# Performance work log

Measured on AMD Instinct MI355X. Metric: run time of the kernel, lower is better.

## Reference

```python
import jax, jax.numpy as jnp
import numpy as np
from jax import lax

V, D, H, L, K = 50257, 1024, 2048, 6, 3
B, S = 4, 2048
EPS = 1.1920929e-07  # torch.finfo(float32).eps (torch RMSNorm default eps=None)


def rmsnorm(x, w):
    return x * lax.rsqrt(jnp.mean(x * x, axis=-1, keepdims=True) + EPS) * w


def depthwise_conv(x, w, b):
    # x: (B,S,D), w: (D,1,K) depthwise kernel, padding='same' as in torch Conv1d
    y = lax.conv_general_dilated(x.transpose(0, 2, 1), w, (1,), 'SAME',
                                 dimension_numbers=('NCH', 'OIH', 'NCH'),
                                 feature_group_count=x.shape[-1])
    return y.transpose(0, 2, 1) + b


def mingru(x, h0, wz, bz, wh, bh, wo, bo):
    # minGRU: z=sigmoid(Wz x), h_tilde=Wh x, h_t=(1-z_t)h_{t-1}+z_t h_tilde_t (parallel scan)
    z = jax.nn.sigmoid(jnp.einsum('bsd,hd->bsh', x, wz) + bz)
    htil = jnp.einsum('bsd,hd->bsh', x, wh) + bh
    a, bc = 1.0 - z, z * htil

    def comb(c1, c2):
        a1, b1 = c1
        a2, b2 = c2
        return a1 * a2, a2 * b1 + b2

    A, Bc = lax.associative_scan(comb, (a, bc), axis=1)
    h = A * h0[:, None, :] + Bc                      # (B,S,H)
    out = jnp.einsum('bsh,dh->bsd', h, wo) + bo      # project back to model dim
    return out, h[:, -1]


def setup_inputs():
    key = jax.random.key(0)
    ks = jax.random.split(key, 16)
    sc = 0.02
    p = {}
    p['x'] = jax.random.randint(ks[0], (B, S), 0, V)
    p['h_prev'] = jax.random.normal(ks[1], (B, L, H), jnp.float32)
    p['emb'] = jax.random.normal(ks[2], (V, D), jnp.float32) * sc
    p['conv_dw_w'] = jax.random.normal(ks[3], (L, D, 1, K), jnp.float32) * sc
    p['conv_dw_b'] = jnp.zeros((L, D), jnp.float32)
    p['conv_pw_w'] = jax.random.normal(ks[4], (L, D, D), jnp.float32) * sc
    p['conv_pw_b'] = jnp.zeros((L, D), jnp.float32)
    p['n1_w'] = jnp.ones((L, D), jnp.float32)
    p['wz'] = jax.random.normal(ks[5], (L, H, D), jnp.float32) * sc
    p['bz'] = jnp.zeros((L, H), jnp.float32)
    p['wh'] = jax.random.normal(ks[6], (L, H, D), jnp.float32) * sc
    p['bh'] = jnp.zeros((L, H), jnp.float32)
    p['wo'] = jax.random.normal(ks[7], (L, D, H), jnp.float32) * sc
    p['bo'] = jnp.zeros((L, D), jnp.float32)
    p['n2_w'] = jnp.ones((L, D), jnp.float32)
    p['f1_w'] = jax.random.normal(ks[8], (L, H, D), jnp.float32) * sc
    p['f1_b'] = jnp.zeros((L, H), jnp.float32)
    p['f2_w'] = jax.random.normal(ks[9], (L, D, H), jnp.float32) * sc
    p['f2_b'] = jnp.zeros((L, D), jnp.float32)
    p['norm_w'] = jnp.ones((D,), jnp.float32)
    p['out_w'] = jax.random.normal(ks[10], (H, D), jnp.float32) * sc
    p['out_b'] = jnp.zeros((H,), jnp.float32)
    return p


def reference(x, h_prev, emb, conv_dw_w, conv_dw_b, conv_pw_w, conv_pw_b, n1_w,
              wz, bz, wh, bh, wo, bo, n2_w, f1_w, f1_b, f2_w, f2_b,
              norm_w, out_w, out_b):
    xe = emb[x]                                      # (B,S,D)
    h_next = []
    for l in range(L):
        c = depthwise_conv(xe, conv_dw_w[l], conv_dw_b[l])
        c = jnp.einsum('bsd,ed->bse', c, conv_pw_w[l]) + conv_pw_b[l]  # 1x1 conv
        xe = c + xe
        g, hl = mingru(rmsnorm(xe, n1_w[l]), h_prev[:, l],
                       wz[l], bz[l], wh[l], bh[l], wo[l], bo[l])
        xe = g + xe
        f = rmsnorm(xe, n2_w[l])
        f = jnp.einsum('bsd,hd->bsh', f, f1_w[l]) + f1_b[l]
        f = jax.nn.gelu(f, approximate=False)
        f = jnp.einsum('bsh,dh->bsd', f, f2_w[l]) + f2_b[l]
        xe = f + xe
        h_next.append(hl)
    out = jnp.einsum('bsd,hd->bsh', rmsnorm(xe, norm_w), out_w) + out_b
    return out, jnp.stack(h_next, axis=1)             # (B,S,H), (B,L,H)
```

## Files before the change

kernel.cpp:

```cpp
#include <hip/hip_runtime.h>

typedef __bf16 bf16x8 __attribute__((ext_vector_type(8)));
typedef float f32x4 __attribute__((ext_vector_type(4)));

#define DEVI __device__ __forceinline__

namespace {
constexpr int cB = 4, cS = 2048, cD = 1024, cH = 2048, cL = 6;
constexpr int cM = cB * cS;
constexpr float cEPS = 1.1920929e-07f;
constexpr int NCH = 16, CHS = cS / NCH;
}

DEVI unsigned short f2bf(float f) {
  union { float f; unsigned u; } c; c.f = f;
  const unsigned u = c.u;
  return (unsigned short)((u + 0x7fffu + ((u >> 16) & 1u)) >> 16);
}
DEVI float bf2f(unsigned short h) {
  union { unsigned u; float f; } c; c.u = ((unsigned)h) << 16;
  return c.f;
}

DEVI void gld16(const void* g, void* l) {
  __builtin_amdgcn_global_load_lds(
      (__attribute__((address_space(1))) void*)g,
      (__attribute__((address_space(3))) void*)l, 16, 0, 0);
}

union F4 { float4 v; float a[4]; };

__global__ __launch_bounds__(256) void embed_k(const int* __restrict__ x,
    const float* __restrict__ emb, float* __restrict__ xe) {
  const int bs = blockIdx.x;
  const int idx = x[bs];
  const int t = threadIdx.x;
  *(float4*)&xe[(size_t)bs * cD + t * 4] =
      *(const float4*)&emb[(size_t)idx * cD + t * 4];
}

__global__ __launch_bounds__(256) void dwconv_k(const float* __restrict__ xe,
    const float* __restrict__ w, const float* __restrict__ bias,
    unsigned short* __restrict__ out) {
  const int bs = blockIdx.x;
  const int s = bs & (cS - 1);
  const int t = threadIdx.x;
  const int d = t * 4;
  const size_t base = (size_t)bs * cD + d;
  F4 x0, xm, xp, vb;
  x0.v = *(const float4*)&xe[base];
  xm.v = make_float4(0.f, 0.f, 0.f, 0.f);
  xp.v = make_float4(0.f, 0.f, 0.f, 0.f);
  if (s > 0) xm.v = *(const float4*)&xe[base - cD];
  if (s < cS - 1) xp.v = *(const float4*)&xe[base + cD];
  vb.v = *(const float4*)&bias[d];
  unsigned short o[4];
#pragma unroll
  for (int j = 0; j < 4; ++j) {
    const float w0 = w[(d + j) * 3 + 0];
    const float w1 = w[(d + j) * 3 + 1];
    const float w2 = w[(d + j) * 3 + 2];
    o[j] = f2bf(xm.a[j] * w0 + x0.a[j] * w1 + xp.a[j] * w2 + vb.a[j]);
  }
  *(ushort4*)&out[base] = make_ushort4(o[0], o[1], o[2], o[3]);
}

__global__ __launch_bounds__(256) void rmsnorm_k(const float* __restrict__ x,
    const float* __restrict__ w, unsigned short* __restrict__ o) {
  const int row = blockIdx.x;
  const int t = threadIdx.x;
  const size_t base = (size_t)row * cD + t * 4;
  F4 v; v.v = *(const float4*)&x[base];
  float ss = v.a[0]*v.a[0] + v.a[1]*v.a[1] + v.a[2]*v.a[2] + v.a[3]*v.a[3];
#pragma unroll
  for (int off = 32; off > 0; off >>= 1) ss += __shfl_down(ss, off, 64);
  __shared__ float red[4];
  if ((t & 63) == 0) red[t >> 6] = ss;
  __syncthreads();
  const float scale = rsqrtf((red[0]+red[1]+red[2]+red[3]) * (1.f/cD) + cEPS);
  F4 wv; wv.v = *(const float4*)&w[t * 4];
  *(ushort4*)&o[base] = make_ushort4(
      f2bf(v.a[0]*scale*wv.a[0]), f2bf(v.a[1]*scale*wv.a[1]),
      f2bf(v.a[2]*scale*wv.a[2]), f2bf(v.a[3]*scale*wv.a[3]));
}

__global__ __launch_bounds__(256) void cvt_k(const float* __restrict__ s,
    unsigned short* __restrict__ d, int n) {
  const int i = (blockIdx.x * 256 + threadIdx.x) * 4;
  if (i >= n) return;
  F4 v; v.v = *(const float4*)&s[i];
  *(ushort4*)&d[i] = make_ushort4(f2bf(v.a[0]), f2bf(v.a[1]),
                                  f2bf(v.a[2]), f2bf(v.a[3]));
}

template<int N, int K, int EPI>
__global__ __launch_bounds__(256) void gemm_bt(
    const unsigned short* __restrict__ A, const unsigned short* __restrict__ W,
    const float* __restrict__ bias, float* __restrict__ Cf,
    unsigned short* __restrict__ Cb) {
  __shared__ unsigned short As[128 * 32];
  __shared__ unsigned short Bs[128 * 32];
  const int t = threadIdx.x;
  const int lane = t & 63;
  const int wave = t >> 6;
  const int m0 = blockIdx.x * 128;
  const int n0 = blockIdx.y * 128;
  const int wm = (wave >> 1) * 64;
  const int wn = (wave & 1) * 64;
  const int fr = lane & 15;
  const int fk = (lane >> 4) * 8;

  const int arow = t >> 2;
  const int acol = (t & 3) * 8;
  const unsigned short* gA = A + (size_t)(m0 + arow) * K + acol;
  const unsigned short* gB = W + (size_t)(n0 + arow) * K + acol;
  unsigned short* lA = As + wave * 512;
  unsigned short* lB = Bs + wave * 512;

  f32x4 acc[4][4] = {};
  for (int k0 = 0; k0 < K; k0 += 32) {
    gld16(gA + k0, lA);
    gld16(gA + k0 + (size_t)64 * K, lA + 2048);
    gld16(gB + k0, lB);
    gld16(gB + k0 + (size_t)64 * K, lB + 2048);
    __syncthreads();
    bf16x8 fa[4], fb[4];
#pragma unroll
    for (int i = 0; i < 4; ++i) {
      fa[i] = *(const bf16x8*)&As[(wm + i * 16 + fr) * 32 + fk];
      fb[i] = *(const bf16x8*)&Bs[(wn + i * 16 + fr) * 32 + fk];
    }
#pragma unroll
    for (int i = 0; i < 4; ++i)
#pragma unroll
      for (int j = 0; j < 4; ++j)
        acc[i][j] = __builtin_amdgcn_mfma_f32_16x16x32_bf16(
            fa[i], fb[j], acc[i][j], 0, 0, 0);
    __syncthreads();
  }

  const int r0 = m0 + wm + ((lane >> 4) << 2);
  const int c0 = n0 + wn + fr;
#pragma unroll
  for (int i = 0; i < 4; ++i)
#pragma unroll
    for (int j = 0; j < 4; ++j) {
      const int col = c0 + j * 16;
      const float bv = bias[col];
#pragma unroll
      for (int r = 0; r < 4; ++r) {
        const size_t idx = (size_t)(r0 + i * 16 + r) * N + col;
        const float v = acc[i][j][r] + bv;
        if constexpr (EPI == 1) {
          Cf[idx] += v;
        } else {
          Cf[idx] = v;
        }
      }
    }
}

#define RDA(BUF, MH)                                                        \
  _Pragma("unroll") for (int mf = 0; mf < 4; ++mf)                          \
  _Pragma("unroll") for (int kk = 0; kk < 2; ++kk)                          \
      a[mf * 2 + kk] = *(const bf16x8*)&lds[(BUF)*16384 + aB + (MH)*4096 +  \
                                            mf * 1024 + kk * 32];

#define RDB(BUF)                                                            \
  _Pragma("unroll") for (int q = 0; q < 4; ++q)                             \
  _Pragma("unroll") for (int kk = 0; kk < 2; ++kk)                          \
      b[q >> 1][(q & 1) * 2 + kk] =                                         \
          *(const bf16x8*)&lds[(BUF)*16384 + bB + q * 1024 + kk * 32];

#define MMQ(MH, NH)                                                         \
  _Pragma("unroll") for (int mf = 0; mf < 4; ++mf)                          \
  _Pragma("unroll") for (int nf = 0; nf < 2; ++nf)                          \
  _Pragma("unroll") for (int kk = 0; kk < 2; ++kk)                          \
      acc[(MH)*4 + mf][(NH)*2 + nf] = __builtin_amdgcn_mfma_f32_16x16x32_bf16( \
          a[mf * 2 + kk], b[NH][nf * 2 + kk], acc[(MH)*4 + mf][(NH)*2 + nf],  \
          0, 0, 0);

#define PH_SYNC()                                                           \
  __builtin_amdgcn_s_barrier();                                             \
  asm volatile("s_waitcnt lgkmcnt(0)" ::: "memory");                        \
  __builtin_amdgcn_sched_barrier(0);                                        \
  __builtin_amdgcn_s_setprio(1)

#define PH_END()                                                            \
  __builtin_amdgcn_s_setprio(0);                                            \
  __builtin_amdgcn_s_barrier()

#define TILE_PHASES(TI, BUF, OBUF)                                          \
  {                                                                         \
    RDA(BUF, 0); RDB(BUF);                                                  \
    { const int n1 = (TI) + 1;                                              \
      stA((n1 < NT) ? n1 : 0, 1, (n1 < NT) ? ldsA(OBUF, 1) : ldsDummy); }   \
    asm volatile("s_waitcnt lgkmcnt(8)" ::: "memory");                      \
    PH_SYNC(); MMQ(0, 0); PH_END();                                         \
    { const int n2 = (TI) + 2;                                              \
      stB((n2 < NT) ? n2 : 0, 0, (n2 < NT) ? ldsB(BUF, 0) : ldsDummy); }    \
    PH_SYNC(); MMQ(0, 1); PH_END();                                         \
    RDA(BUF, 1);                                                            \
    { const int n2 = (TI) + 2;                                              \
      stB((n2 < NT) ? n2 : 0, 1, (n2 < NT) ? ldsB(BUF, 1) : ldsDummy); }    \
    PH_SYNC(); MMQ(1, 1); PH_END();                                         \
    { const int n2 = (TI) + 2;                                              \
      stA((n2 < NT) ? n2 : 0, 0, (n2 < NT) ? ldsA(BUF, 0) : ldsDummy); }    \
    asm volatile("s_waitcnt vmcnt(6)" ::: "memory");                        \
    PH_SYNC(); MMQ(1, 0); PH_END();                                         \
  }

template<int N, int K, int EPI, int NS>
__global__ __launch_bounds__(512, 2) void gemm8p(
    const unsigned short* __restrict__ A,
    const unsigned short* __restrict__ W0,
    const unsigned short* __restrict__ W1,
    const float* __restrict__ bias0, const float* __restrict__ bias1,
    float* __restrict__ Cf, unsigned short* __restrict__ Cb,
    unsigned short* __restrict__ Cb2) {
  static_assert(K % 128 == 0, "NT must be even");
  constexpr int NT = K / 64;
  __shared__ unsigned short lds[73728];
  const int t = threadIdx.x;
  const int lane = t & 63;
  const int wave = t >> 6;
  const int wr = wave >> 2;
  const int wc = wave & 3;
  const int m0 = blockIdx.x * 256;
  const int n0 = blockIdx.y * 256;

  const bool zpart = (n0 < NS);
  const unsigned short* Wp = zpart ? W0 : W1;
  const int nw0 = zpart ? n0 : n0 - NS;
  const float* bp = zpart ? bias0 : bias1;
  const int CW = zpart ? NS : (N - NS);

  const int srow = t >> 3;
  const int scol = ((t & 7) * 8) ^ (((t >> 5) & 1) << 4);
  const unsigned short* gA = A  + (size_t)(m0 + srow) * K + scol;
  const unsigned short* gB = Wp + (size_t)(nw0 + srow) * K + scol;
  const int ldsw = wave * 512;

  auto ldsA = [&](int buf, int h) -> unsigned short* {
    return (unsigned short*)&lds[buf * 16384 + h * 8192 + ldsw];
  };
  auto ldsB = [&](int buf, int h) -> unsigned short* {
    return (unsigned short*)&lds[32768 + buf * 16384 + h * 8192 + ldsw];
  };
  unsigned short* ldsDummy = (unsigned short*)&lds[65536 + ldsw];
  auto stA = [&](int tile, int h, unsigned short* dst) {
    const unsigned short* s = gA + (size_t)(h * 128) * K + tile * 64;
    gld16(s, dst);
    gld16(s + (size_t)64 * K, dst + 4096);
  };
  auto stB = [&](int tile, int h, unsigned short* dst) {
    const unsigned short* s = gB + (size_t)(h * 128) * K + tile * 64;
    gld16(s, dst);
    gld16(s + (size_t)64 * K, dst + 4096);
  };

  const int sx = ((lane >> 2) & 1) << 4;
  const int aoff = (lane & 15) * 64 + (((lane >> 4) * 8) ^ sx);
  const int aB = wr * 8192 + aoff;
  const int bB = 32768 + (wc >> 1) * 8192 + (wc & 1) * 4096 + aoff;

  bf16x8 a[8];
  bf16x8 b[2][4];
  f32x4 acc[8][4] = {};

  stB(0, 0, ldsB(0, 0)); stB(0, 1, ldsB(0, 1));
  stA(0, 0, ldsA(0, 0)); stA(0, 1, ldsA(0, 1));
  stB(1, 0, ldsB(1, 0)); stB(1, 1, ldsB(1, 1));
  stA(1, 0, ldsA(1, 0));
  asm volatile("s_waitcnt vmcnt(6)" ::: "memory");
  __builtin_amdgcn_s_barrier();

  for (int tp = 0; tp < NT / 2; ++tp) {
    const int t0 = 2 * tp;
    TILE_PHASES(t0, 0, 1);
    TILE_PHASES(t0 + 1, 1, 0);
  }

  float* cf = Cf;
  unsigned short* cb = zpart ? Cb : Cb2;
  const int r0 = m0 + wr * 128 + ((lane >> 4) << 2);
  const int c0 = nw0 + wc * 64 + (lane & 15);
#pragma unroll
  for (int mfg = 0; mfg < 8; ++mfg) {
#pragma unroll
    for (int nfg = 0; nfg < 4; ++nfg) {
      const int col = c0 + nfg * 16;
      const float bv = bp[col];
#pragma unroll
      for (int r = 0; r < 4; ++r) {
        const size_t idx = (size_t)(r0 + mfg * 16 + r) * CW + col;
        const float v = acc[mfg][nfg][r] + bv;
        if constexpr (EPI == 0) {
          cf[idx] = v;
        } else if constexpr (EPI == 4) {
          cb[idx] = f2bf(0.5f * v * (1.f + erff(v * 0.70710678118654752f)));
        } else {
          if (zpart) cb[idx] = f2bf(1.f / (1.f + __expf(-v)));
          else       cb[idx] = f2bf(v);
        }
      }
    }
  }
}

__global__ __launch_bounds__(256) void scan1_k(const unsigned short* __restrict__ z,
    const unsigned short* __restrict__ ht, float* __restrict__ Ac,
    float* __restrict__ Bc) {
  const int tid = blockIdx.x * 256 + threadIdx.x;
  const int hp = (tid & (cH / 2 - 1)) * 2;
  const int ck = (tid / (cH / 2)) & (NCH - 1);
  const int b = tid / ((cH / 2) * NCH);
  const size_t base = ((size_t)b * cS + (size_t)ck * CHS) * cH + hp;
  float a0 = 1.f, s0 = 0.f, a1 = 1.f, s1 = 0.f;
#pragma unroll 4
  for (int s = 0; s < CHS; ++s) {
    const unsigned zz = *(const unsigned*)&z[base + (size_t)s * cH];
    const unsigned hh = *(const unsigned*)&ht[base + (size_t)s * cH];
    const float z0 = bf2f((unsigned short)(zz & 0xffff)), z1 = bf2f((unsigned short)(zz >> 16));
    const float t0 = bf2f((unsigned short)(hh & 0xffff)), t1 = bf2f((unsigned short)(hh >> 16));
    const float aa0 = 1.f - z0, aa1 = 1.f - z1;
    s0 = aa0 * s0 + z0 * t0; a0 *= aa0;
    s1 = aa1 * s1 + z1 * t1; a1 *= aa1;
  }
  const size_t so = ((size_t)b * NCH + ck) * cH + hp;
  *(float2*)&Ac[so] = make_float2(a0, a1);
  *(float2*)&Bc[so] = make_float2(s0, s1);
}

__global__ __launch_bounds__(256) void scan2_k(const float* __restrict__ Ac,
    const float* __restrict__ Bc, const float* __restrict__ h_prev,
    float* __restrict__ P, float* __restrict__ hn, int l) {
  const int tid = blockIdx.x * 256 + threadIdx.x;
  const int h = tid & (cH - 1);
  const int b = tid >> 11;
  float run = h_prev[((size_t)b * cL + l) * cH + h];
#pragma unroll
  for (int c = 0; c < NCH; ++c) {
    const size_t so = ((size_t)b * NCH + c) * cH + h;
    P[so] = run;
    run = Ac[so] * run + Bc[so];
  }
  hn[((size_t)b * cL + l) * cH + h] = run;
}

__global__ __launch_bounds__(256) void scan3_k(const unsigned short* __restrict__ z,
    unsigned short* __restrict__ ht, const float* __restrict__ P) {
  const int tid = blockIdx.x * 256 + threadIdx.x;
  const int hp = (tid & (cH / 2 - 1)) * 2;
  const int ck = (tid / (cH / 2)) & (NCH - 1);
  const int b = tid / ((cH / 2) * NCH);
  const size_t base = ((size_t)b * cS + (size_t)ck * CHS) * cH + hp;
  const size_t so = ((size_t)b * NCH + ck) * cH + hp;
  const float2 rr = *(const float2*)&P[so];
  float r0 = rr.x, r1 = rr.y;
#pragma unroll 4
  for (int s = 0; s < CHS; ++s) {
    const unsigned zz = *(const unsigned*)&z[base + (size_t)s * cH];
    const unsigned hh = *(const unsigned*)&ht[base + (size_t)s * cH];
    const float z0 = bf2f((unsigned short)(zz & 0xffff)), z1 = bf2f((unsigned short)(zz >> 16));
    const float t0 = bf2f((unsigned short)(hh & 0xffff)), t1 = bf2f((unsigned short)(hh >> 16));
    r0 = (1.f - z0) * r0 + z0 * t0;
    r1 = (1.f - z1) * r1 + z1 * t1;
    *(unsigned*)&ht[base + (size_t)s * cH] =
        (unsigned)f2bf(r0) | ((unsigned)f2bf(r1) << 16);
  }
}

extern "C" void kernel_launch(void* const* d_in, const int* in_sizes, int n_in,
                              void* d_out, int out_size, void* d_ws, size_t ws_size,
                              hipStream_t stream) {
  (void)in_sizes; (void)n_in; (void)out_size; (void)ws_size;
  const int*   x      = (const int*)d_in[0];
  const float* h_prev = (const float*)d_in[1];
  const float* emb    = (const float*)d_in[2];
  const float* cdw_w  = (const float*)d_in[3];
  const float* cdw_b  = (const float*)d_in[4];
  const float* cpw_w  = (const float*)d_in[5];
  const float* cpw_b  = (const float*)d_in[6];
  const float* n1w    = (const float*)d_in[7];
  const float* wzp    = (const float*)d_in[8];
  const float* bzp    = (const float*)d_in[9];
  const float* whp    = (const float*)d_in[10];
  const float* bhp    = (const float*)d_in[11];
  const float* wop    = (const float*)d_in[12];
  const float* bop    = (const float*)d_in[13];
  const float* n2w    = (const float*)d_in[14];
  const float* f1wp   = (const float*)d_in[15];
  const float* f1bp   = (const float*)d_in[16];
  const float* f2wp   = (const float*)d_in[17];
  const float* f2bp   = (const float*)d_in[18];
  const float* nw     = (const float*)d_in[19];
  const float* owp    = (const float*)d_in[20];
  const float* obp    = (const float*)d_in[21];

  float* out_main = (float*)d_out;
  float* out_hn   = out_main + (size_t)cM * cH;

  char* p = (char*)d_ws;
  auto alloc = [&](size_t bytes) {
    char* r = p; p += (bytes + 255) & ~(size_t)255; return r;
  };
  float*          xe = (float*)alloc((size_t)cM * cD * 4);
  unsigned short* xn = (unsigned short*)alloc((size_t)cM * cD * 2);
  unsigned short* zb = (unsigned short*)alloc((size_t)cM * cH * 2);
  unsigned short* hb = (unsigned short*)alloc((size_t)cM * cH * 2);
  float* Ac = (float*)alloc((size_t)cB * NCH * cH * 4);
  float* Bc = (float*)alloc((size_t)cB * NCH * cH * 4);
  float* Pr = (float*)alloc((size_t)cB * NCH * cH * 4);
  unsigned short* w_pw = (unsigned short*)alloc((size_t)cL * cD * cD * 2);
  unsigned short* w_z  = (unsigned short*)alloc((size_t)cL * cH * cD * 2);
  unsigned short* w_h  = (unsigned short*)alloc((size_t)cL * cH * cD * 2);
  unsigned short* w_o  = (unsigned short*)alloc((size_t)cL * cD * cH * 2);
  unsigned short* w_f1 = (unsigned short*)alloc((size_t)cL * cH * cD * 2);
  unsigned short* w_f2 = (unsigned short*)alloc((size_t)cL * cD * cH * 2);
  unsigned short* w_ow = (unsigned short*)alloc((size_t)cH * cD * 2);

  auto cvt = [&](const float* src, unsigned short* dst, size_t n) {
    cvt_k<<<dim3((unsigned)(n / 1024)), 256, 0, stream>>>(src, dst, (int)n);
  };

  cvt(cpw_w, w_pw, (size_t)cL * cD * cD);
  cvt(wzp,  w_z,  (size_t)cL * cH * cD);
  cvt(whp,  w_h,  (size_t)cL * cH * cD);
  cvt(wop,  w_o,  (size_t)cL * cD * cH);
  cvt(f1wp, w_f1, (size_t)cL * cH * cD);
  cvt(f2wp, w_f2, (size_t)cL * cD * cH);
  cvt(owp,  w_ow, (size_t)cH * cD);

  embed_k<<<cM, 256, 0, stream>>>(x, emb, xe);

  for (int l = 0; l < cL; ++l) {
    const size_t oDD = (size_t)l * cD * cD, oHD = (size_t)l * cH * cD;

    dwconv_k<<<cM, 256, 0, stream>>>(xe, cdw_w + (size_t)l * cD * 3,
                                     cdw_b + (size_t)l * cD, xn);
    gemm_bt<cD, cD, 1><<<dim3(cM / 128, cD / 128), 256, 0, stream>>>(
        xn, w_pw + oDD, cpw_b + (size_t)l * cD, xe, nullptr);

    rmsnorm_k<<<cM, 256, 0, stream>>>(xe, n1w + (size_t)l * cD, xn);
    gemm8p<2 * cH, cD, 5, cH><<<dim3(cM / 256, 2 * cH / 256), 512, 0, stream>>>(
        xn, w_z + oHD, w_h + oHD, bzp + (size_t)l * cH, bhp + (size_t)l * cH,
        nullptr, zb, hb);
    scan1_k<<<cB * NCH * (cH / 2) / 256, 256, 0, stream>>>(zb, hb, Ac, Bc);
    scan2_k<<<cB * cH / 256, 256, 0, stream>>>(Ac, Bc, h_prev, Pr, out_hn, l);
    scan3_k<<<cB * NCH * (cH / 2) / 256, 256, 0, stream>>>(zb, hb, Pr);
    gemm_bt<cD, cH, 1><<<dim3(cM / 128, cD / 128), 256, 0, stream>>>(
        hb, w_o + oHD, bop + (size_t)l * cD, xe, nullptr);

    rmsnorm_k<<<cM, 256, 0, stream>>>(xe, n2w + (size_t)l * cD, xn);
    gemm8p<cH, cD, 4, cH><<<dim3(cM / 256, cH / 256), 512, 0, stream>>>(
        xn, w_f1 + oHD, w_f1 + oHD, f1bp + (size_t)l * cH, f1bp + (size_t)l * cH,
        nullptr, zb, zb);
    gemm_bt<cD, cH, 1><<<dim3(cM / 128, cD / 128), 256, 0, stream>>>(
        zb, w_f2 + oHD, f2bp + (size_t)l * cD, xe, nullptr);
  }

  rmsnorm_k<<<cM, 256, 0, stream>>>(xe, nw, xn);
  gemm8p<cH, cD, 0, cH><<<dim3(cM / 256, cH / 256), 512, 0, stream>>>(
      xn, w_ow, w_ow, obp, obp, out_main, nullptr, nullptr);
}
```

Measured before the change: 2.359 ms.

## Peel GEMM tail tiles, stage bf16 epilogue through LDS, fuse scan passes

The 256x256 GEMM main loop now peels its last two tiles so out-of-range prefetches into a dummy LDS region are no longer issued. This shrinks shared memory and splits the B-fragment reads across phases. The bf16 epilogues write through swizzled LDS and then issue coalesced 16-byte global stores instead of scattered 2-byte stores. The scan's carry-propagation and apply kernels are merged: each chunk thread recomputes its prefix from the per-chunk A/B summaries, which removes one launch and the P buffer at the cost of redundant serial prefix work. The reordered prologue loads and changed wait counts must still match the pipeline's outstanding-load accounting.

```diff
diff --git a/kernel.cpp b/kernel.cpp
--- a/kernel.cpp
+++ b/kernel.cpp
@@ -166,10 +166,15 @@
       a[mf * 2 + kk] = *(const bf16x8*)&lds[(BUF)*16384 + aB + (MH)*4096 +  \
                                             mf * 1024 + kk * 32];
 
-#define RDB(BUF)                                                            \
-  _Pragma("unroll") for (int q = 0; q < 4; ++q)                             \
+#define RDB0(BUF)                                                           \
+  _Pragma("unroll") for (int q = 0; q < 2; ++q)                             \
   _Pragma("unroll") for (int kk = 0; kk < 2; ++kk)                          \
-      b[q >> 1][(q & 1) * 2 + kk] =                                         \
+      b[0][q * 2 + kk] = *(const bf16x8*)&lds[(BUF)*16384 + bB + q * 1024 + kk * 32];
+
+#define RDB1(BUF)                                                           \
+  _Pragma("unroll") for (int q = 2; q < 4; ++q)                             \
+  _Pragma("unroll") for (int kk = 0; kk < 2; ++kk)                          \
+      b[1][(q & 1) * 2 + kk] =                                              \
           *(const bf16x8*)&lds[(BUF)*16384 + bB + q * 1024 + kk * 32];
 
 #define MMQ(MH, NH)                                                         \
@@ -190,23 +195,19 @@
   __builtin_amdgcn_s_setprio(0);                                            \
   __builtin_amdgcn_s_barrier()
 
-#define TILE_PHASES(TI, BUF, OBUF)                                          \
+#define TILE_PHASES(TI, BUF, OBUF, S1, S2, VM)                              \
   {                                                                         \
-    RDA(BUF, 0); RDB(BUF);                                                  \
-    { const int n1 = (TI) + 1;                                              \
-      stA((n1 < NT) ? n1 : 0, 1, (n1 < NT) ? ldsA(OBUF, 1) : ldsDummy); }   \
-    asm volatile("s_waitcnt lgkmcnt(8)" ::: "memory");                      \
+    RDA(BUF, 0); RDB0(BUF);                                                 \
+    if (S1) { stA((TI) + 1, 1, ldsA(OBUF, 1)); }                            \
     PH_SYNC(); MMQ(0, 0); PH_END();                                         \
-    { const int n2 = (TI) + 2;                                              \
-      stB((n2 < NT) ? n2 : 0, 0, (n2 < NT) ? ldsB(BUF, 0) : ldsDummy); }    \
+    RDB1(BUF);                                                              \
     PH_SYNC(); MMQ(0, 1); PH_END();                                         \
     RDA(BUF, 1);                                                            \
-    { const int n2 = (TI) + 2;                                              \
-      stB((n2 < NT) ? n2 : 0, 1, (n2 < NT) ? ldsB(BUF, 1) : ldsDummy); }    \
+    if (S2) { stB((TI) + 2, 0, ldsB(BUF, 0)); }                             \
     PH_SYNC(); MMQ(1, 1); PH_END();                                         \
-    { const int n2 = (TI) + 2;                                              \
-      stA((n2 < NT) ? n2 : 0, 0, (n2 < NT) ? ldsA(BUF, 0) : ldsDummy); }    \
-    asm volatile("s_waitcnt vmcnt(6)" ::: "memory");                        \
+    if (S2) { stB((TI) + 2, 1, ldsB(BUF, 1)); stA((TI) + 2, 0, ldsA(BUF, 0)); } \
+    if (VM == 6) { asm volatile("s_waitcnt vmcnt(6)" ::: "memory"); }       \
+    else         { asm volatile("s_waitcnt vmcnt(0)" ::: "memory"); }       \
     PH_SYNC(); MMQ(1, 0); PH_END();                                         \
   }
 
@@ -220,7 +221,7 @@
     unsigned short* __restrict__ Cb2) {
   static_assert(K % 128 == 0, "NT must be even");
   constexpr int NT = K / 64;
-  __shared__ unsigned short lds[73728];
+  __shared__ unsigned short lds[65536];
   const int t = threadIdx.x;
   const int lane = t & 63;
   const int wave = t >> 6;
@@ -247,7 +248,6 @@
   auto ldsB = [&](int buf, int h) -> unsigned short* {
     return (unsigned short*)&lds[32768 + buf * 16384 + h * 8192 + ldsw];
   };
-  unsigned short* ldsDummy = (unsigned short*)&lds[65536 + ldsw];
   auto stA = [&](int tile, int h, unsigned short* dst) {
     const unsigned short* s = gA + (size_t)(h * 128) * K + tile * 64;
     gld16(s, dst);
@@ -268,42 +268,65 @@
   bf16x8 b[2][4];
   f32x4 acc[8][4] = {};
 
+  stA(0, 0, ldsA(0, 0)); stA(0, 1, ldsA(0, 1));
   stB(0, 0, ldsB(0, 0)); stB(0, 1, ldsB(0, 1));
-  stA(0, 0, ldsA(0, 0)); stA(0, 1, ldsA(0, 1));
+  stA(1, 0, ldsA(1, 0));
   stB(1, 0, ldsB(1, 0)); stB(1, 1, ldsB(1, 1));
-  stA(1, 0, ldsA(1, 0));
   asm volatile("s_waitcnt vmcnt(6)" ::: "memory");
   __builtin_amdgcn_s_barrier();
 
-  for (int tp = 0; tp < NT / 2; ++tp) {
+  for (int tp = 0; tp < NT / 2 - 1; ++tp) {
     const int t0 = 2 * tp;
-    TILE_PHASES(t0, 0, 1);
-    TILE_PHASES(t0 + 1, 1, 0);
-  }
-
-  float* cf = Cf;
-  unsigned short* cb = zpart ? Cb : Cb2;
-  const int r0 = m0 + wr * 128 + ((lane >> 4) << 2);
-  const int c0 = nw0 + wc * 64 + (lane & 15);
-#pragma unroll
-  for (int mfg = 0; mfg < 8; ++mfg) {
-#pragma unroll
-    for (int nfg = 0; nfg < 4; ++nfg) {
-      const int col = c0 + nfg * 16;
-      const float bv = bp[col];
-#pragma unroll
-      for (int r = 0; r < 4; ++r) {
-        const size_t idx = (size_t)(r0 + mfg * 16 + r) * CW + col;
-        const float v = acc[mfg][nfg][r] + bv;
-        if constexpr (EPI == 0) {
-          cf[idx] = v;
-        } else if constexpr (EPI == 4) {
-          cb[idx] = f2bf(0.5f * v * (1.f + erff(v * 0.70710678118654752f)));
-        } else {
-          if (zpart) cb[idx] = f2bf(1.f / (1.f + __expf(-v)));
-          else       cb[idx] = f2bf(v);
+    TILE_PHASES(t0, 0, 1, 1, 1, 6);
+    TILE_PHASES(t0 + 1, 1, 0, 1, 1, 6);
+  }
+  TILE_PHASES(NT - 2, 0, 1, 1, 0, 0);
+  TILE_PHASES(NT - 1, 1, 0, 0, 0, 0);
+
+  const int r0l = wr * 128 + ((lane >> 4) << 2);
+  const int c0l = wc * 64 + (lane & 15);
+  if constexpr (EPI == 0) {
+    const int r0 = m0 + r0l;
+    const int c0 = nw0 + c0l;
+#pragma unroll
+    for (int mfg = 0; mfg < 8; ++mfg)
+#pragma unroll
+      for (int nfg = 0; nfg < 4; ++nfg) {
+        const int col = c0 + nfg * 16;
+        const float bv = bp[col];
+#pragma unroll
+        for (int r = 0; r < 4; ++r)
+          Cf[(size_t)(r0 + mfg * 16 + r) * CW + col] = acc[mfg][nfg][r] + bv;
+      }
+  } else {
+    unsigned short* cb = zpart ? Cb : Cb2;
+#pragma unroll
+    for (int mfg = 0; mfg < 8; ++mfg)
+#pragma unroll
+      for (int nfg = 0; nfg < 4; ++nfg) {
+        const int col = c0l + nfg * 16;
+        const float bv = bp[nw0 + col];
+#pragma unroll
+        for (int r = 0; r < 4; ++r) {
+          const float v = acc[mfg][nfg][r] + bv;
+          unsigned short o;
+          if constexpr (EPI == 4) {
+            o = f2bf(0.5f * v * (1.f + erff(v * 0.70710678118654752f)));
+          } else {
+            o = zpart ? f2bf(1.f / (1.f + __expf(-v))) : f2bf(v);
+          }
+          const int rr = r0l + mfg * 16 + r;
+          lds[rr * 256 + (col ^ (((rr >> 2) & 3) << 4))] = o;
         }
       }
+    __syncthreads();
+#pragma unroll
+    for (int it = 0; it < 16; ++it) {
+      const int flat = it * 512 + t;
+      const int row = flat >> 5;
+      const int ch = flat & 31;
+      const float4 v = *(const float4*)&lds[row * 256 + ((ch * 8) ^ (((row >> 2) & 3) << 4))];
+      *(float4*)&cb[(size_t)(m0 + row) * CW + nw0 + ch * 8] = v;
     }
   }
 }
@@ -332,32 +355,25 @@
   *(float2*)&Bc[so] = make_float2(s0, s1);
 }
 
-__global__ __launch_bounds__(256) void scan2_k(const float* __restrict__ Ac,
+__global__ __launch_bounds__(256) void scan23_k(const unsigned short* __restrict__ z,
+    unsigned short* __restrict__ ht, const float* __restrict__ Ac,
     const float* __restrict__ Bc, const float* __restrict__ h_prev,
-    float* __restrict__ P, float* __restrict__ hn, int l) {
-  const int tid = blockIdx.x * 256 + threadIdx.x;
-  const int h = tid & (cH - 1);
-  const int b = tid >> 11;
-  float run = h_prev[((size_t)b * cL + l) * cH + h];
-#pragma unroll
-  for (int c = 0; c < NCH; ++c) {
-    const size_t so = ((size_t)b * NCH + c) * cH + h;
-    P[so] = run;
-    run = Ac[so] * run + Bc[so];
-  }
-  hn[((size_t)b * cL + l) * cH + h] = run;
-}
-
-__global__ __launch_bounds__(256) void scan3_k(const unsigned short* __restrict__ z,
-    unsigned short* __restrict__ ht, const float* __restrict__ P) {
+    float* __restrict__ hn, int l) {
   const int tid = blockIdx.x * 256 + threadIdx.x;
   const int hp = (tid & (cH / 2 - 1)) * 2;
   const int ck = (tid / (cH / 2)) & (NCH - 1);
   const int b = tid / ((cH / 2) * NCH);
+  const size_t hoff = ((size_t)b * cL + l) * cH + hp;
+  const float2 h0 = *(const float2*)&h_prev[hoff];
+  float r0 = h0.x, r1 = h0.y;
+  for (int c = 0; c < ck; ++c) {
+    const size_t so = ((size_t)b * NCH + c) * cH + hp;
+    const float2 av = *(const float2*)&Ac[so];
+    const float2 bv = *(const float2*)&Bc[so];
+    r0 = av.x * r0 + bv.x;
+    r1 = av.y * r1 + bv.y;
+  }
   const size_t base = ((size_t)b * cS + (size_t)ck * CHS) * cH + hp;
-  const size_t so = ((size_t)b * NCH + ck) * cH + hp;
-  const float2 rr = *(const float2*)&P[so];
-  float r0 = rr.x, r1 = rr.y;
 #pragma unroll 4
   for (int s = 0; s < CHS; ++s) {
     const unsigned zz = *(const unsigned*)&z[base + (size_t)s * cH];
@@ -369,6 +385,7 @@
     *(unsigned*)&ht[base + (size_t)s * cH] =
         (unsigned)f2bf(r0) | ((unsigned)f2bf(r1) << 16);
   }
+  if (ck == NCH - 1) *(float2*)&hn[hoff] = make_float2(r0, r1);
 }
 
 extern "C" void kernel_launch(void* const* d_in, const int* in_sizes, int n_in,
@@ -411,7 +428,6 @@
   unsigned short* hb = (unsigned short*)alloc((size_t)cM * cH * 2);
   float* Ac = (float*)alloc((size_t)cB * NCH * cH * 4);
   float* Bc = (float*)alloc((size_t)cB * NCH * cH * 4);
-  float* Pr = (float*)alloc((size_t)cB * NCH * cH * 4);
   unsigned short* w_pw = (unsigned short*)alloc((size_t)cL * cD * cD * 2);
   unsigned short* w_z  = (unsigned short*)alloc((size_t)cL * cH * cD * 2);
   unsigned short* w_h  = (unsigned short*)alloc((size_t)cL * cH * cD * 2);
@@ -447,8 +463,8 @@
         xn, w_z + oHD, w_h + oHD, bzp + (size_t)l * cH, bhp + (size_t)l * cH,
         nullptr, zb, hb);
     scan1_k<<<cB * NCH * (cH / 2) / 256, 256, 0, stream>>>(zb, hb, Ac, Bc);
-    scan2_k<<<cB * cH / 256, 256, 0, stream>>>(Ac, Bc, h_prev, Pr, out_hn, l);
-    scan3_k<<<cB * NCH * (cH / 2) / 256, 256, 0, stream>>>(zb, hb, Pr);
+    scan23_k<<<cB * NCH * (cH / 2) / 256, 256, 0, stream>>>(zb, hb, Ac, Bc,
+                                                            h_prev, out_hn, l);
     gemm_bt<cD, cH, 1><<<dim3(cM / 128, cD / 128), 256, 0, stream>>>(
         hb, w_o + oHD, bop + (size_t)l * cD, xe, nullptr);
 
```

After: 2.387 ms. Within noise of the previous version (+1.2%).
